# Optimization experiments

Measured on AMD Instinct MI355X. Metric: run time of the kernel, lower is better.

The kernel has to match this reference:

```python
import jax, jax.numpy as jnp
import numpy as np
from jax import lax

LATENT = 1024
EMB, AUD, VIS = 300, 74, 35
D = EMB + AUD + VIS  # 409


def _uniform(key, shape, k):
    return jax.random.uniform(key, shape, jnp.float32, -k, k)


def setup_inputs() -> dict:
    key = jax.random.key(0)
    ks = jax.random.split(key, 12)
    B, T, H = 64, 256, LATENT
    k = 1.0 / np.sqrt(H)
    inp = {
        "inputs": jax.random.normal(ks[0], (B, T, D), jnp.float32),
        # encoder LSTM params (torch layout: [4H, in], gate order i,f,g,o)
        "enc_Wih": _uniform(ks[1], (4 * H, D), k),
        "enc_Whh": _uniform(ks[2], (4 * H, H), k),
        "enc_b": _uniform(ks[3], (4 * H,), k) + _uniform(ks[4], (4 * H,), k),
        # decoder LSTM params
        "dec_Wih": _uniform(ks[5], (4 * H, D), k),
        "dec_Whh": _uniform(ks[6], (4 * H, H), k),
        "dec_b": _uniform(ks[7], (4 * H,), k) + _uniform(ks[8], (4 * H,), k),
        # prediction head
        "pred_W": _uniform(ks[9], (D, H), k),
        "pred_b": _uniform(ks[10], (D,), k),
    }
    return inp


def _lstm(x_tbd, h0, c0, Wih, Whh, b):
    """Single-layer LSTM over time-major x [T,B,Din]. Returns (hs [T,B,H], hT, cT)."""
    def step(carry, x_t):
        h, c = carry
        g = x_t @ Wih.T + h @ Whh.T + b  # [B,4H]
        i, f, gg, o = jnp.split(g, 4, axis=-1)
        c = jax.nn.sigmoid(f) * c + jax.nn.sigmoid(i) * jnp.tanh(gg)
        h = jax.nn.sigmoid(o) * jnp.tanh(c)
        return (h, c), h
    (hT, cT), hs = lax.scan(step, (h0, c0), x_tbd)
    return hs, hT, cT


def reference(inputs, enc_Wih, enc_Whh, enc_b, dec_Wih, dec_Whh, dec_b, pred_W, pred_b):
    x = jnp.transpose(inputs, (1, 0, 2))  # [T,B,D] time-major
    T, B, _ = x.shape
    H = enc_Whh.shape[1]
    z = jnp.zeros((B, H), x.dtype)
    _, hT, cT = _lstm(x, z, z, enc_Wih, enc_Whh, enc_b)
    latents = hT[None]  # [1,B,H], matches torch (num_layers=1)
    # Decoder input at step i is zeros for i=0, else inputs[i-1] (teacher forcing),
    # so the whole decode is one ordinary LSTM pass over the shifted sequence.
    dec_in = jnp.concatenate([jnp.zeros((1, B, x.shape[2]), x.dtype), x[:-1]], axis=0)
    hs, _, _ = _lstm(dec_in, hT, cT, dec_Wih, dec_Whh, dec_b)
    seq = hs @ pred_W.T + pred_b  # [T,B,D]
    seq = jnp.transpose(seq, (1, 0, 2))  # [B,T,D]
    return (latents, seq)
```

## Files before the change

kernel.cpp:

```cpp
#include <hip/hip_runtime.h>

#define B_ 64
#define T_ 256
#define H_ 1024
#define D_ 409
#define NWG 256
#define NSLOT 513

typedef _Float16 h8 __attribute__((ext_vector_type(8)));
typedef float f4 __attribute__((ext_vector_type(4)));
typedef unsigned u4v __attribute__((ext_vector_type(4)));

__device__ __forceinline__ float sigf(float x) {
  return 1.f / (1.f + __expf(-x));
}
__device__ __forceinline__ float tanhf_(float x) {
  return 1.f - 2.f / (1.f + __expf(2.f * x));
}

__global__ __launch_bounds__(256) void prep_kernel(
    const float* __restrict__ inp, const float* __restrict__ Pw,
    _Float16* __restrict__ xP, _Float16* __restrict__ PP,
    int* __restrict__ flags)
{
  const int NX = 256 * 4 * 13 * 64;
  const int NP = 26 * 32 * 64;
  int gid = blockIdx.x * 256 + threadIdx.x;
  if (gid < NWG) flags[gid] = 0;
  if (gid < NX) {
    int lane = gid & 63; int q = gid >> 6;
    int kc = q % 13; q /= 13;
    int mt = q & 3;  int t = q >> 2;
    const float* src = inp + ((size_t)(16 * mt + (lane & 15)) * T_ + t) * D_;
    int k0 = kc * 32 + 8 * (lane >> 4);
    h8 v;
#pragma unroll
    for (int e = 0; e < 8; ++e) {
      int k = k0 + e;
      v[e] = (k < D_) ? (_Float16)src[k] : (_Float16)0.f;
    }
    *(h8*)(xP + (size_t)gid * 8) = v;
  } else if (gid < NX + NP) {
    int r = gid - NX;
    int lane = r & 63; int q = r >> 6;
    int kc = q & 31; int nt = q >> 5;
    int n = nt * 16 + (lane & 15);
    int k0 = kc * 32 + 8 * (lane >> 4);
    h8 v;
#pragma unroll
    for (int e = 0; e < 8; ++e)
      v[e] = (n < D_) ? (_Float16)Pw[(size_t)n * H_ + k0 + e] : (_Float16)0.f;
    *(h8*)(PP + (size_t)r * 8) = v;
  }
}

#define H_ISS(KC, OFFB) \
  asm volatile( \
    "global_load_dwordx4 %0, %4, %8 offset:" #OFFB "\n\t" \
    "global_load_dwordx4 %1, %5, %8 offset:" #OFFB "\n\t" \
    "global_load_dwordx4 %2, %6, %8 offset:" #OFFB "\n\t" \
    "global_load_dwordx4 %3, %7, %8 offset:" #OFFB "\n\t" \
    : "=&v"(BH[KC][0]), "=&v"(BH[KC][1]), "=&v"(BH[KC][2]), "=&v"(BH[KC][3]) \
    : "v"(va0), "v"(va1), "v"(va2), "v"(va3), "s"(hb) \
    : "memory")

#define HWAIT(N) do { \
  asm volatile("s_waitcnt vmcnt(" #N ")" ::: "memory"); \
  __builtin_amdgcn_sched_barrier(0); \
} while (0)

#define HCONS(KC) do { \
  _Pragma("unroll") \
  for (int mt_ = 0; mt_ < 4; ++mt_) { \
    h8 av_ = __builtin_bit_cast(h8, BH[KC][mt_]); \
    acc[mt_] = __builtin_amdgcn_mfma_f32_16x16x32_f16(av_, Whi[KC], acc[mt_], 0, 0, 0); \
    acc[mt_] = __builtin_amdgcn_mfma_f32_16x16x32_f16(av_, Wlo[KC], acc[mt_], 0, 0, 0); \
  } \
} while (0)

__global__ __launch_bounds__(256, 1) void recur_kernel(
    const float* __restrict__ eWhh, const float* __restrict__ eb,
    const float* __restrict__ dWhh, const float* __restrict__ db,
    const float* __restrict__ eWih, const float* __restrict__ dWih,
    const _Float16* __restrict__ xP, _Float16* __restrict__ ring,
    int* __restrict__ flags, float* __restrict__ latents)
{
  __shared__ float red[4 * 64 * 20];

  const int tid  = threadIdx.x;
  const int w    = blockIdx.x;
  const int m    = tid >> 6;
  const int lane = tid & 63;
  const int ci   = lane & 15;
  const int q    = lane >> 4;
  const int uu   = ci >> 2, g = ci & 3;
  const int nrow = g * H_ + 4 * w + uu;
  const int eb_  = tid >> 2, euu = tid & 3;

  h8 Whi[8], Wlo[8], Ihi[4], Ilo[4];
  float bias4[4];
  float c_reg = 0.f;
  const int kbeg = (m == 0) ? 0 : (3 * m + 1);
  const int kend = 3 * m + 4;
  const int nkc  = kend - kbeg;

  const unsigned colb = (unsigned)((m * 256 + 8 * q) * 2);
  const unsigned va0 = (unsigned)(ci * H_ * 2) + colb;
  const unsigned va1 = va0 + 16 * H_ * 2;
  const unsigned va2 = va1 + 16 * H_ * 2;
  const unsigned va3 = va2 + 16 * H_ * 2;

#pragma unroll 1
  for (int s = 1; s <= 512; ++s) {
    if (s == 1 || s == 257) {
      const float* Whh = (s == 1) ? eWhh : dWhh;
      const float* Wih = (s == 1) ? eWih : dWih;
      const float* bb  = (s == 1) ? eb : db;
#pragma unroll
      for (int kc = 0; kc < 8; ++kc) {
        const float* p = Whh + (size_t)nrow * H_ + m * 256 + kc * 32 + 8 * q;
#pragma unroll
        for (int e = 0; e < 8; ++e) {
          float wf = p[e];
          _Float16 hi = (_Float16)wf;
          Whi[kc][e] = hi;
          Wlo[kc][e] = (_Float16)(wf - (float)hi);
        }
      }
      for (int j = 0; j < 4; ++j) {
        if (j < nkc) {
          int kc = kbeg + j;
          int k0 = kc * 32 + 8 * q;
#pragma unroll
          for (int e = 0; e < 8; ++e) {
            int k = k0 + e;
            float wf = (k < D_) ? Wih[(size_t)nrow * D_ + k] : 0.f;
            _Float16 hi = (_Float16)wf;
            Ihi[j][e] = hi;
            Ilo[j][e] = (_Float16)(wf - (float)hi);
          }
        }
      }
#pragma unroll
      for (int g2 = 0; g2 < 4; ++g2)
        bias4[g2] = bb[g2 * H_ + 4 * w + euu];
    }

    const bool have_h = (s > 1);
    const int  t_x    = (s <= 256) ? (s - 1) : (s - 258);
    const bool have_x = (t_x >= 0);

    f4 acc[4];
#pragma unroll
    for (int mt = 0; mt < 4; ++mt) { f4 z = {0.f, 0.f, 0.f, 0.f}; acc[mt] = z; }

    if (have_x) {
      for (int j = 0; j < 4; ++j) {
        if (j < nkc) {
          int kc = kbeg + j;
#pragma unroll
          for (int mt = 0; mt < 4; ++mt) {
            h8 a = *(const h8*)(xP + ((size_t)((t_x * 4 + mt) * 13 + kc) * 64 + lane) * 8);
            acc[mt] = __builtin_amdgcn_mfma_f32_16x16x32_f16(a, Ihi[j], acc[mt], 0, 0, 0);
            acc[mt] = __builtin_amdgcn_mfma_f32_16x16x32_f16(a, Ilo[j], acc[mt], 0, 0, 0);
          }
        }
      }
    }

    if (have_h) {
      asm volatile("s_waitcnt vmcnt(0)" ::: "memory");
      {
        int* fp = flags + 64 * m + lane;
        const int target = s - 1;
        int it = 0;
        while (__hip_atomic_load(fp, __ATOMIC_RELAXED, __HIP_MEMORY_SCOPE_AGENT) < target) {
          if (++it > (1 << 20)) break;
        }
      }
      asm volatile("" ::: "memory");

      const _Float16* hb = ring + (size_t)(s - 1) * (B_ * H_);
      u4v BH[8][4];
      H_ISS(0, 0);   H_ISS(1, 64);  H_ISS(2, 128); H_ISS(3, 192);
      H_ISS(4, 256); H_ISS(5, 320); H_ISS(6, 384); H_ISS(7, 448);
      HWAIT(28); HCONS(0);
      HWAIT(24); HCONS(1);
      HWAIT(20); HCONS(2);
      HWAIT(16); HCONS(3);
      HWAIT(12); HCONS(4);
      HWAIT(8);  HCONS(5);
      HWAIT(4);  HCONS(6);
      HWAIT(0);  HCONS(7);
    }

#pragma unroll
    for (int mt = 0; mt < 4; ++mt)
#pragma unroll
      for (int r = 0; r < 4; ++r)
        red[(m * 64 + 16 * mt + 4 * q + r) * 20 + ci] = acc[mt][r];
    __syncthreads();

    f4 sum = *(const f4*)(&red[(0 * 64 + eb_) * 20 + 4 * euu]);
#pragma unroll
    for (int mv = 1; mv < 4; ++mv)
      sum += *(const f4*)(&red[(mv * 64 + eb_) * 20 + 4 * euu]);
    float gi = sum[0] + bias4[0];
    float gf = sum[1] + bias4[1];
    float gg = sum[2] + bias4[2];
    float go = sum[3] + bias4[3];
    float cold = have_h ? c_reg : 0.f;
    float cn = sigf(gf) * cold + sigf(gi) * tanhf_(gg);
    float hn = sigf(go) * tanhf_(cn);
    c_reg = cn;
    _Float16 h16 = (_Float16)hn;
    unsigned short h16u = __builtin_bit_cast(unsigned short, h16);
    __hip_atomic_store(
        (unsigned short*)(ring + (size_t)s * (B_ * H_) + (size_t)eb_ * H_ + 4 * w + euu),
        h16u, __ATOMIC_RELAXED, __HIP_MEMORY_SCOPE_AGENT);
    if (s == 256)
      latents[(size_t)eb_ * H_ + 4 * w + euu] = hn;

    asm volatile("s_waitcnt vmcnt(0)" ::: "memory");
    __syncthreads();
    if (tid == 0)
      __hip_atomic_store(flags + w, s, __ATOMIC_RELAXED, __HIP_MEMORY_SCOPE_AGENT);
  }
}

__global__ __launch_bounds__(256) void pred_kernel(
    const _Float16* __restrict__ hs, const _Float16* __restrict__ PP,
    const float* __restrict__ pb, float* __restrict__ outseq)
{
  int wt = blockIdx.x * 4 + (threadIdx.x >> 6);
  int lane = threadIdx.x & 63;
  int nt = wt % 26, mt = wt / 26;
  int i = lane & 15, q = lane >> 4;
  int n = nt * 16 + i;
  float bias = (n < D_) ? pb[n] : 0.f;
  f4 acc = {bias, bias, bias, bias};
  int R = mt * 16;
#pragma unroll 4
  for (int kc = 0; kc < 32; ++kc) {
    h8 a = *(const h8*)(hs + (size_t)(R + i) * H_ + kc * 32 + 8 * q);
    h8 b = *(const h8*)(PP + ((size_t)(nt * 32 + kc) * 64 + lane) * 8);
    acc = __builtin_amdgcn_mfma_f32_16x16x32_f16(a, b, acc, 0, 0, 0);
  }
#pragma unroll
  for (int r = 0; r < 4; ++r) {
    int row = R + 4 * q + r;
    int t = row >> 6, bb = row & 63;
    if (n < D_) outseq[((size_t)bb * T_ + t) * D_ + n] = acc[r];
  }
}

extern "C" void kernel_launch(void* const* d_in, const int* in_sizes, int n_in,
                              void* d_out, int out_size, void* d_ws, size_t ws_size,
                              hipStream_t stream) {
  const float* inp  = (const float*)d_in[0];
  const float* eWih = (const float*)d_in[1];
  const float* eWhh = (const float*)d_in[2];
  const float* eb   = (const float*)d_in[3];
  const float* dWih = (const float*)d_in[4];
  const float* dWhh = (const float*)d_in[5];
  const float* db   = (const float*)d_in[6];
  const float* pW   = (const float*)d_in[7];
  const float* pb   = (const float*)d_in[8];
  float* out = (float*)d_out;
  float* latents = out;
  float* seq = out + 64 * 1024;

  char* ws = (char*)d_ws;
  size_t off = 0;
  auto alloc = [&](size_t bytes) {
    void* p = ws + off;
    off = (off + bytes + 255) & ~(size_t)255;
    return p;
  };
  _Float16* xP   = (_Float16*)alloc((size_t)256 * 4 * 13 * 64 * 8 * 2);
  _Float16* PP   = (_Float16*)alloc((size_t)26 * 32 * 64 * 8 * 2);
  _Float16* ring = (_Float16*)alloc((size_t)NSLOT * B_ * H_ * 2);
  int* flags     = (int*)alloc(NWG * 4);

  hipLaunchKernelGGL(prep_kernel, dim3(3536), dim3(256), 0, stream,
                     inp, pW, xP, PP, flags);
  hipLaunchKernelGGL(recur_kernel, dim3(NWG), dim3(256), 0, stream,
                     eWhh, eb, dWhh, db, eWih, dWih, xP, ring, flags, latents);
  hipLaunchKernelGGL(pred_kernel, dim3(6656), dim3(256), 0, stream,
                     ring + (size_t)257 * B_ * H_, PP, pb, seq);
}
```

Measured before the change: 3.671 ms.

## Repartition recurrent LSTM so each wave owns full-K tiles with per-wave flags

Reassigns work in the persistent recurrent kernel so each wavefront owns a 16-batch by 4-unit tile over the full hidden dimension. Each wave then holds all 32 K-chunks of Whh in registers, which removes the LDS cross-wave reduction and both __syncthreads per step. Synchronisation moves from one flag per workgroup to per-wave flags polled with vector loads, and the input projection is prefetched before the wait with the Wih low half dropped. The costs are much higher register pressure, four times more flags to poll, and lower precision on the input projection.

```diff
diff --git a/kernel.cpp b/kernel.cpp
--- a/kernel.cpp
+++ b/kernel.cpp
@@ -4,12 +4,13 @@
 #define T_ 256
 #define H_ 1024
 #define D_ 409
-#define NWG 256
+#define NFLAG 1024
 #define NSLOT 513
 
 typedef _Float16 h8 __attribute__((ext_vector_type(8)));
 typedef float f4 __attribute__((ext_vector_type(4)));
 typedef unsigned u4v __attribute__((ext_vector_type(4)));
+typedef int i4v __attribute__((ext_vector_type(4)));
 
 __device__ __forceinline__ float sigf(float x) {
   return 1.f / (1.f + __expf(-x));
@@ -26,7 +27,7 @@
   const int NX = 256 * 4 * 13 * 64;
   const int NP = 26 * 32 * 64;
   int gid = blockIdx.x * 256 + threadIdx.x;
-  if (gid < NWG) flags[gid] = 0;
+  if (gid < NFLAG) flags[gid] = 0;
   if (gid < NX) {
     int lane = gid & 63; int q = gid >> 6;
     int kc = q % 13; q /= 13;
@@ -54,27 +55,27 @@
   }
 }
 
-#define H_ISS(KC, OFFB) \
-  asm volatile( \
-    "global_load_dwordx4 %0, %4, %8 offset:" #OFFB "\n\t" \
-    "global_load_dwordx4 %1, %5, %8 offset:" #OFFB "\n\t" \
-    "global_load_dwordx4 %2, %6, %8 offset:" #OFFB "\n\t" \
-    "global_load_dwordx4 %3, %7, %8 offset:" #OFFB "\n\t" \
-    : "=&v"(BH[KC][0]), "=&v"(BH[KC][1]), "=&v"(BH[KC][2]), "=&v"(BH[KC][3]) \
-    : "v"(va0), "v"(va1), "v"(va2), "v"(va3), "s"(hb) \
-    : "memory")
-
-#define HWAIT(N) do { \
+#define VMW(N) do { \
   asm volatile("s_waitcnt vmcnt(" #N ")" ::: "memory"); \
   __builtin_amdgcn_sched_barrier(0); \
 } while (0)
 
-#define HCONS(KC) do { \
+#define HISS(G, O0, O1, O2, O3) \
+  asm volatile( \
+    "global_load_dwordx4 %0, %4, %5 offset:" #O0 "\n\t" \
+    "global_load_dwordx4 %1, %4, %5 offset:" #O1 "\n\t" \
+    "global_load_dwordx4 %2, %4, %5 offset:" #O2 "\n\t" \
+    "global_load_dwordx4 %3, %4, %5 offset:" #O3 "\n\t" \
+    : "=&v"(BH[(G) & 3][0]), "=&v"(BH[(G) & 3][1]), \
+      "=&v"(BH[(G) & 3][2]), "=&v"(BH[(G) & 3][3]) \
+    : "v"(voff_h), "s"(hb) : "memory")
+
+#define HCONS(G) do { \
   _Pragma("unroll") \
-  for (int mt_ = 0; mt_ < 4; ++mt_) { \
-    h8 av_ = __builtin_bit_cast(h8, BH[KC][mt_]); \
-    acc[mt_] = __builtin_amdgcn_mfma_f32_16x16x32_f16(av_, Whi[KC], acc[mt_], 0, 0, 0); \
-    acc[mt_] = __builtin_amdgcn_mfma_f32_16x16x32_f16(av_, Wlo[KC], acc[mt_], 0, 0, 0); \
+  for (int i_ = 0; i_ < 4; ++i_) { \
+    h8 hv_ = __builtin_bit_cast(h8, BH[(G) & 3][i_]); \
+    accP[i_] = __builtin_amdgcn_mfma_f32_16x16x32_f16(Whi[4 * (G) + i_], hv_, accP[i_], 0, 0, 0); \
+    accP[i_] = __builtin_amdgcn_mfma_f32_16x16x32_f16(Wlo[4 * (G) + i_], hv_, accP[i_], 0, 0, 0); \
   } \
 } while (0)
 
@@ -85,30 +86,28 @@
     const _Float16* __restrict__ xP, _Float16* __restrict__ ring,
     int* __restrict__ flags, float* __restrict__ latents)
 {
-  __shared__ float red[4 * 64 * 20];
-
   const int tid  = threadIdx.x;
   const int w    = blockIdx.x;
-  const int m    = tid >> 6;
+  const int mw   = tid >> 6;
   const int lane = tid & 63;
   const int ci   = lane & 15;
   const int q    = lane >> 4;
-  const int uu   = ci >> 2, g = ci & 3;
-  const int nrow = g * H_ + 4 * w + uu;
-  const int eb_  = tid >> 2, euu = tid & 3;
-
-  h8 Whi[8], Wlo[8], Ihi[4], Ilo[4];
-  float bias4[4];
+  const int r16  = (w & 7) >> 1;
+  const int u16  = ((w >> 3) << 1) | (w & 1);
+  const int ubase = u16 * 16 + mw * 4;
+  const int wr   = (ci & 3) * H_ + ubase + (ci >> 2);
+  const int brow = 16 * r16 + ci;
+  const int uout = ubase + q;
+  const int fidx = r16 * 256 + u16 * 4 + mw;
+
+  const unsigned voff_h  = (unsigned)((brow * H_ + 8 * q) * 2);
+  const unsigned voff_st = (unsigned)((brow * H_ + uout) * 2);
+  const unsigned voff_f  = (unsigned)(r16 * 1024 + lane * 16);
+  const unsigned voff_x  = (unsigned)(lane * 16);
+
+  h8 Whi[32], Wlo[32], Ih[13];
+  f4 bias4;
   float c_reg = 0.f;
-  const int kbeg = (m == 0) ? 0 : (3 * m + 1);
-  const int kend = 3 * m + 4;
-  const int nkc  = kend - kbeg;
-
-  const unsigned colb = (unsigned)((m * 256 + 8 * q) * 2);
-  const unsigned va0 = (unsigned)(ci * H_ * 2) + colb;
-  const unsigned va1 = va0 + 16 * H_ * 2;
-  const unsigned va2 = va1 + 16 * H_ * 2;
-  const unsigned va3 = va2 + 16 * H_ * 2;
 
 #pragma unroll 1
   for (int s = 1; s <= 512; ++s) {
@@ -116,9 +115,9 @@
       const float* Whh = (s == 1) ? eWhh : dWhh;
       const float* Wih = (s == 1) ? eWih : dWih;
       const float* bb  = (s == 1) ? eb : db;
-#pragma unroll
-      for (int kc = 0; kc < 8; ++kc) {
-        const float* p = Whh + (size_t)nrow * H_ + m * 256 + kc * 32 + 8 * q;
+#pragma unroll 4
+      for (int kc = 0; kc < 32; ++kc) {
+        const float* p = Whh + (size_t)wr * H_ + kc * 32 + 8 * q;
 #pragma unroll
         for (int e = 0; e < 8; ++e) {
           float wf = p[e];
@@ -127,104 +126,117 @@
           Wlo[kc][e] = (_Float16)(wf - (float)hi);
         }
       }
-      for (int j = 0; j < 4; ++j) {
-        if (j < nkc) {
-          int kc = kbeg + j;
-          int k0 = kc * 32 + 8 * q;
-#pragma unroll
-          for (int e = 0; e < 8; ++e) {
-            int k = k0 + e;
-            float wf = (k < D_) ? Wih[(size_t)nrow * D_ + k] : 0.f;
-            _Float16 hi = (_Float16)wf;
-            Ihi[j][e] = hi;
-            Ilo[j][e] = (_Float16)(wf - (float)hi);
-          }
+#pragma unroll
+      for (int kc = 0; kc < 13; ++kc) {
+        int k0 = kc * 32 + 8 * q;
+#pragma unroll
+        for (int e = 0; e < 8; ++e) {
+          int k = k0 + e;
+          Ih[kc][e] = (k < D_) ? (_Float16)Wih[(size_t)wr * D_ + k] : (_Float16)0.f;
         }
       }
 #pragma unroll
-      for (int g2 = 0; g2 < 4; ++g2)
-        bias4[g2] = bb[g2 * H_ + 4 * w + euu];
+      for (int g2 = 0; g2 < 4; ++g2) bias4[g2] = bb[g2 * H_ + uout];
+      asm volatile("s_waitcnt vmcnt(0)" ::: "memory");
     }
 
     const bool have_h = (s > 1);
     const int  t_x    = (s <= 256) ? (s - 1) : (s - 258);
     const bool have_x = (t_x >= 0);
 
-    f4 acc[4];
-#pragma unroll
-    for (int mt = 0; mt < 4; ++mt) { f4 z = {0.f, 0.f, 0.f, 0.f}; acc[mt] = z; }
-
+    f4 accP[4], accX[2];
+#pragma unroll
+    for (int j = 0; j < 4; ++j) { f4 z = {0.f, 0.f, 0.f, 0.f}; accP[j] = z; }
+    accX[0] = accP[0]; accX[1] = accP[0];
+
+    u4v xB[13];
     if (have_x) {
-      for (int j = 0; j < 4; ++j) {
-        if (j < nkc) {
-          int kc = kbeg + j;
-#pragma unroll
-          for (int mt = 0; mt < 4; ++mt) {
-            h8 a = *(const h8*)(xP + ((size_t)((t_x * 4 + mt) * 13 + kc) * 64 + lane) * 8);
-            acc[mt] = __builtin_amdgcn_mfma_f32_16x16x32_f16(a, Ihi[j], acc[mt], 0, 0, 0);
-            acc[mt] = __builtin_amdgcn_mfma_f32_16x16x32_f16(a, Ilo[j], acc[mt], 0, 0, 0);
-          }
-        }
+      const _Float16* xb0 = xP + ((size_t)(t_x * 4 + r16) * 13 + 0) * 512;
+      const _Float16* xb1 = xb0 + 4 * 512;
+      const _Float16* xb2 = xb0 + 8 * 512;
+      const _Float16* xb3 = xb0 + 12 * 512;
+      asm volatile(
+        "global_load_dwordx4 %0, %13, %14\n\t"
+        "global_load_dwordx4 %1, %13, %14 offset:1024\n\t"
+        "global_load_dwordx4 %2, %13, %14 offset:2048\n\t"
+        "global_load_dwordx4 %3, %13, %14 offset:3072\n\t"
+        "global_load_dwordx4 %4, %13, %15\n\t"
+        "global_load_dwordx4 %5, %13, %15 offset:1024\n\t"
+        "global_load_dwordx4 %6, %13, %15 offset:2048\n\t"
+        "global_load_dwordx4 %7, %13, %15 offset:3072\n\t"
+        "global_load_dwordx4 %8, %13, %16\n\t"
+        "global_load_dwordx4 %9, %13, %16 offset:1024\n\t"
+        "global_load_dwordx4 %10, %13, %16 offset:2048\n\t"
+        "global_load_dwordx4 %11, %13, %16 offset:3072\n\t"
+        "global_load_dwordx4 %12, %13, %17\n\t"
+        : "=&v"(xB[0]), "=&v"(xB[1]), "=&v"(xB[2]), "=&v"(xB[3]),
+          "=&v"(xB[4]), "=&v"(xB[5]), "=&v"(xB[6]), "=&v"(xB[7]),
+          "=&v"(xB[8]), "=&v"(xB[9]), "=&v"(xB[10]), "=&v"(xB[11]),
+          "=&v"(xB[12])
+        : "v"(voff_x), "s"(xb0), "s"(xb1), "s"(xb2), "s"(xb3)
+        : "memory");
+    }
+
+    if (s > 1) {
+      if (have_x) { VMW(13); } else { VMW(0); }
+      if (lane == 0)
+        __hip_atomic_store(flags + fidx, s - 1, __ATOMIC_RELAXED,
+                           __HIP_MEMORY_SCOPE_AGENT);
+    }
+
+    if (have_x) {
+      if (s > 1) { VMW(1); } else { VMW(0); }
+#pragma unroll
+      for (int kc = 0; kc < 13; ++kc) {
+        h8 xv = __builtin_bit_cast(h8, xB[kc]);
+        accX[kc & 1] = __builtin_amdgcn_mfma_f32_16x16x32_f16(Ih[kc], xv, accX[kc & 1], 0, 0, 0);
       }
     }
 
     if (have_h) {
-      asm volatile("s_waitcnt vmcnt(0)" ::: "memory");
-      {
-        int* fp = flags + 64 * m + lane;
-        const int target = s - 1;
-        int it = 0;
-        while (__hip_atomic_load(fp, __ATOMIC_RELAXED, __HIP_MEMORY_SCOPE_AGENT) < target) {
-          if (++it > (1 << 20)) break;
-        }
+      const int target = s - 1;
+      int it = 0;
+      while (true) {
+        i4v fv;
+        asm volatile("global_load_dwordx4 %0, %1, %2 sc0 sc1\n\t"
+                     "s_waitcnt vmcnt(0)"
+                     : "=v"(fv) : "v"(voff_f), "s"(flags) : "memory");
+        int mn0 = fv[0] < fv[1] ? fv[0] : fv[1];
+        int mn1 = fv[2] < fv[3] ? fv[2] : fv[3];
+        int mn = mn0 < mn1 ? mn0 : mn1;
+        if (!__any(mn < target)) break;
+        if (++it > (1 << 14)) break;
       }
-      asm volatile("" ::: "memory");
+      __builtin_amdgcn_sched_barrier(0);
 
       const _Float16* hb = ring + (size_t)(s - 1) * (B_ * H_);
-      u4v BH[8][4];
-      H_ISS(0, 0);   H_ISS(1, 64);  H_ISS(2, 128); H_ISS(3, 192);
-      H_ISS(4, 256); H_ISS(5, 320); H_ISS(6, 384); H_ISS(7, 448);
-      HWAIT(28); HCONS(0);
-      HWAIT(24); HCONS(1);
-      HWAIT(20); HCONS(2);
-      HWAIT(16); HCONS(3);
-      HWAIT(12); HCONS(4);
-      HWAIT(8);  HCONS(5);
-      HWAIT(4);  HCONS(6);
-      HWAIT(0);  HCONS(7);
-    }
-
-#pragma unroll
-    for (int mt = 0; mt < 4; ++mt)
-#pragma unroll
-      for (int r = 0; r < 4; ++r)
-        red[(m * 64 + 16 * mt + 4 * q + r) * 20 + ci] = acc[mt][r];
-    __syncthreads();
-
-    f4 sum = *(const f4*)(&red[(0 * 64 + eb_) * 20 + 4 * euu]);
-#pragma unroll
-    for (int mv = 1; mv < 4; ++mv)
-      sum += *(const f4*)(&red[(mv * 64 + eb_) * 20 + 4 * euu]);
-    float gi = sum[0] + bias4[0];
-    float gf = sum[1] + bias4[1];
-    float gg = sum[2] + bias4[2];
-    float go = sum[3] + bias4[3];
+      u4v BH[4][4];
+      HISS(0, 0, 64, 128, 192);
+      HISS(1, 256, 320, 384, 448);
+      HISS(2, 512, 576, 640, 704);
+      HISS(3, 768, 832, 896, 960);
+      VMW(12); HCONS(0); HISS(4, 1024, 1088, 1152, 1216);
+      VMW(12); HCONS(1); HISS(5, 1280, 1344, 1408, 1472);
+      VMW(12); HCONS(2); HISS(6, 1536, 1600, 1664, 1728);
+      VMW(12); HCONS(3); HISS(7, 1792, 1856, 1920, 1984);
+      VMW(12); HCONS(4);
+      VMW(8);  HCONS(5);
+      VMW(4);  HCONS(6);
+      VMW(0);  HCONS(7);
+    }
+
+    f4 tot = accP[0] + accP[1] + accP[2] + accP[3] + accX[0] + accX[1] + bias4;
     float cold = have_h ? c_reg : 0.f;
-    float cn = sigf(gf) * cold + sigf(gi) * tanhf_(gg);
-    float hn = sigf(go) * tanhf_(cn);
+    float cn = sigf(tot[1]) * cold + sigf(tot[0]) * tanhf_(tot[2]);
+    float hn = sigf(tot[3]) * tanhf_(cn);
     c_reg = cn;
     _Float16 h16 = (_Float16)hn;
-    unsigned short h16u = __builtin_bit_cast(unsigned short, h16);
+    unsigned short hu = __builtin_bit_cast(unsigned short, h16);
     __hip_atomic_store(
-        (unsigned short*)(ring + (size_t)s * (B_ * H_) + (size_t)eb_ * H_ + 4 * w + euu),
-        h16u, __ATOMIC_RELAXED, __HIP_MEMORY_SCOPE_AGENT);
+        (unsigned short*)(ring + (size_t)s * (B_ * H_)) + (brow * H_ + uout),
+        hu, __ATOMIC_RELAXED, __HIP_MEMORY_SCOPE_AGENT);
     if (s == 256)
-      latents[(size_t)eb_ * H_ + 4 * w + euu] = hn;
-
-    asm volatile("s_waitcnt vmcnt(0)" ::: "memory");
-    __syncthreads();
-    if (tid == 0)
-      __hip_atomic_store(flags + w, s, __ATOMIC_RELAXED, __HIP_MEMORY_SCOPE_AGENT);
+      latents[brow * H_ + uout] = hn;
   }
 }
 
@@ -280,11 +292,11 @@
   _Float16* xP   = (_Float16*)alloc((size_t)256 * 4 * 13 * 64 * 8 * 2);
   _Float16* PP   = (_Float16*)alloc((size_t)26 * 32 * 64 * 8 * 2);
   _Float16* ring = (_Float16*)alloc((size_t)NSLOT * B_ * H_ * 2);
-  int* flags     = (int*)alloc(NWG * 4);
+  int* flags     = (int*)alloc(NFLAG * 4);
 
   hipLaunchKernelGGL(prep_kernel, dim3(3536), dim3(256), 0, stream,
                      inp, pW, xP, PP, flags);
-  hipLaunchKernelGGL(recur_kernel, dim3(NWG), dim3(256), 0, stream,
+  hipLaunchKernelGGL(recur_kernel, dim3(256), dim3(256), 0, stream,
                      eWhh, eb, dWhh, db, eWih, dWih, xP, ring, flags, latents);
   hipLaunchKernelGGL(pred_kernel, dim3(6656), dim3(256), 0, stream,
                      ring + (size_t)257 * B_ * H_, PP, pb, seq);
```

Result: slower. 9.747 ms (+165.5%).
